# Kernel tuning notes

Measured on AMD Instinct MI355X. Metric: run time of the kernel, lower is better.

Reference implementation:

```python
import jax, jax.numpy as jnp
from jax import lax
import numpy as np

D = 8        # domain_num
L = 12       # label_num
C = 9        # attr_num
W = 128      # window_size
B = 4096
EPS = 1e-5


def setup_inputs() -> dict:
    key = jax.random.key(0)
    ks = jax.random.split(key, 12)
    s = 0.05
    return {
        "x": jax.random.normal(ks[0], (B, C, 1, W), dtype=jnp.float32),
        "weights": jax.random.uniform(ks[1], (B, D), dtype=jnp.float32),
        # per-domain stacked parameters (leading dim D)
        "gamma": jnp.ones((D, C), dtype=jnp.float32),
        "beta": jnp.zeros((D, C), dtype=jnp.float32),
        "w1": jax.random.normal(ks[2], (D, 32, C, 9), dtype=jnp.float32) * s,
        "b1": jax.random.normal(ks[3], (D, 32), dtype=jnp.float32) * s,
        "w2": jax.random.normal(ks[4], (D, 64, 32, 9), dtype=jnp.float32) * s,
        "b2": jax.random.normal(ks[5], (D, 64), dtype=jnp.float32) * s,
        "fcw": jax.random.normal(ks[6], (D, L, 64 * 26), dtype=jnp.float32) * s,
        "fcb": jax.random.normal(ks[7], (D, L), dtype=jnp.float32) * s,
    }


def _maxpool2(h):
    # MaxPool along width, kernel 2 stride 2 (height is 1 and already squeezed)
    b, c, w = h.shape
    return h.reshape(b, c, w // 2, 2).max(axis=-1)


def _branch(x3, gamma, beta, w1, b1, w2, b2, fcw, fcb):
    # x3: [B, C, W]. BatchNorm2d in training mode: batch stats over (N, H, W).
    mean = x3.mean(axis=(0, 2), keepdims=True)
    var = x3.var(axis=(0, 2), keepdims=True)
    xn = (x3 - mean) * lax.rsqrt(var + EPS) * gamma[None, :, None] + beta[None, :, None]
    dn = ('NCH', 'OIH', 'NCH')
    h = lax.conv_general_dilated(xn, w1, (1,), 'VALID', dimension_numbers=dn)
    h = _maxpool2(jax.nn.relu(h + b1[None, :, None]))          # [B,32,60]
    h = lax.conv_general_dilated(h, w2, (1,), 'VALID', dimension_numbers=dn)
    h = _maxpool2(jax.nn.relu(h + b2[None, :, None]))          # [B,64,26]
    flat = h.reshape(h.shape[0], 64 * 26)
    return jax.nn.relu(flat @ fcw.T + fcb)                      # [B,L]


def reference(x, weights, gamma, beta, w1, b1, w2, b2, fcw, fcb):
    x3 = x[:, :, 0, :]  # squeeze height=1 -> [B,C,W]
    per_domain = jax.vmap(_branch, in_axes=(None, 0, 0, 0, 0, 0, 0, 0, 0))(
        x3, gamma, beta, w1, b1, w2, b2, fcw, fcb)              # [D,B,L]
    # vectorized form of the nested python-loop weighted sum over domains
    return jnp.einsum('bd,dbl->bl', weights, per_domain)        # [B,L]
```

## Files before the change

kernel.cpp:

```cpp
#include <hip/hip_runtime.h>
#include <hip/hip_bf16.h>

#define D 8
#define L 12
#define C 9
#define W 128
#define B 4096
#define EPS 1e-5f

typedef __attribute__((ext_vector_type(8))) short v8s;
typedef __attribute__((ext_vector_type(4))) float v4f;

#define OFF_STATS 0
#define OFF_B1E   1152
#define OFF_W1T   1408
#define OFF_W2T   21888
#define OFF_FCWP  95616

#define REGION 2336

__device__ inline unsigned short f2bf(float f) {
    unsigned u = __builtin_bit_cast(unsigned, f);
    u += 0x7FFFu + ((u >> 16) & 1u);
    return (unsigned short)(u >> 16);
}
__device__ inline unsigned pk2(float a, float b) {
    float2 f2; f2.x = a; f2.y = b;
    __hip_bfloat162 h = __float22bfloat162_rn(f2);
    unsigned u; __builtin_memcpy(&u, &h, 4);
    return u;
}

__global__ void stats_repack_kernel(const float* __restrict__ x,
                                    const float* __restrict__ w2,
                                    const float* __restrict__ fcw,
                                    float* __restrict__ ws,
                                    float* __restrict__ out) {
    const int t = threadIdx.x;
    __shared__ float redS[8];
    if (blockIdx.x < 576) {
        const int c = blockIdx.x % 9;
        const int slice = blockIdx.x / 9;
        const int w4 = t & 31, br = t >> 5;
        const float4* x4 = (const float4*)x;
        float s = 0.f, s2 = 0.f;
        for (int b = slice * 8 + br; b < B; b += 64 * 8) {
            float4 v = x4[(size_t)b * 288 + c * 32 + w4];
            s  += v.x + v.y + v.z + v.w;
            s2 += v.x * v.x + v.y * v.y + v.z * v.z + v.w * v.w;
        }
        for (int off = 32; off >= 1; off >>= 1) {
            s  += __shfl_down(s, off);
            s2 += __shfl_down(s2, off);
        }
        if ((t & 63) == 0) { redS[(t >> 6) * 2] = s; redS[(t >> 6) * 2 + 1] = s2; }
        __syncthreads();
        if (t == 0) {
            ws[OFF_STATS + slice * 18 + c]     = redS[0] + redS[2] + redS[4] + redS[6];
            ws[OFF_STATS + slice * 18 + 9 + c] = redS[1] + redS[3] + redS[5] + redS[7];
        }
    } else if (blockIdx.x < 616) {
        const int i0 = blockIdx.x - 576;
        const int d = i0 / 5, part = i0 % 5;
        short* w2t  = (short*)(ws + OFF_W2T);
        short* fcwp = (short*)(ws + OFF_FCWP);
        if (part < 2) {
            for (int i = part * 256 + t; i < 64 * 9 * 32; i += 512) {
                int o = i / 288, r = i % 288, tap = r / 32, ic = r & 31;
                w2t[(size_t)d * 18432 + i] =
                    (short)f2bf(w2[(((size_t)(d * 64 + o)) * 32 + ic) * 9 + tap]);
            }
        } else {
            for (int i = (part - 2) * 256 + t; i < 12 * 1664; i += 768) {
                int l = i / 1664, k = i % 1664, p = k >> 6, o = k & 63;
                fcwp[((size_t)d * 12) * 1664 + i] =
                    (short)f2bf(fcw[((size_t)(d * 12 + l)) * 1664 + o * 26 + p]);
            }
        }
    } else {
        const int base = (blockIdx.x - 616) * 6144;
        float4 z; z.x = z.y = z.z = z.w = 0.f;
        float4* o4 = (float4*)(out + base);
        for (int i = t; i < 1536; i += 256) o4[i] = z;
    }
}

__global__ void fold1_kernel(const float* __restrict__ w1, const float* __restrict__ b1,
                             const float* __restrict__ gamma, const float* __restrict__ beta,
                             float* __restrict__ ws) {
    const int d = blockIdx.x, t = threadIdx.x;
    __shared__ float g[9], bt[9];
    if (t < 64) {
        for (int c = 0; c < 9; c++) {
            float s  = ws[OFF_STATS + t * 18 + c];
            float s2 = ws[OFF_STATS + t * 18 + 9 + c];
            for (int off = 32; off >= 1; off >>= 1) {
                s  += __shfl_down(s, off);
                s2 += __shfl_down(s2, off);
            }
            if (t == 0) {
                const float N = (float)B * (float)W;
                float m  = s / N;
                float vv = s2 / N - m * m;
                float inv = rsqrtf(vv + EPS);
                float gg = gamma[d * 9 + c] * inv;
                g[c] = gg; bt[c] = beta[d * 9 + c] - gg * m;
            }
        }
    }
    __syncthreads();
    const int o = t >> 3, sub = t & 7;
    short* w1t = (short*)(ws + OFF_W1T);
    short* dst = w1t + (size_t)d * 5120 + o * 160;
    const float* src = w1 + ((size_t)(d * 32 + o)) * 81;
    float bias_part = 0.f;
    for (int tap = sub; tap < 10; tap += 8) {
        for (int c = 0; c < 16; c++) {
            float v = 0.f;
            if (tap < 9 && c < 9) {
                float wv = src[c * 9 + tap];
                v = wv * g[c];
                bias_part += wv * bt[c];
            }
            dst[tap * 16 + c] = (short)f2bf(v);
        }
    }
    bias_part += __shfl_xor(bias_part, 1);
    bias_part += __shfl_xor(bias_part, 2);
    bias_part += __shfl_xor(bias_part, 4);
    if (sub == 0) ws[OFF_B1E + d * 32 + o] = b1[d * 32 + o] + bias_part;
}

__global__ __launch_bounds__(256, 4)
void branch_kernel(const float* __restrict__ x,
                   const float* __restrict__ b2g,
                   const float* __restrict__ fcb,
                   const float* __restrict__ wts,
                   const float* __restrict__ ws,
                   float* __restrict__ out) {
    const int t = threadIdx.x;
    const int lane = t & 63;
    const int wv = t >> 6;
    const int d = blockIdx.y;
    const int b0 = blockIdx.x * 4;
    const short* w1t  = (const short*)(ws + OFF_W1T) + (size_t)d * 5120;
    const short* w2t  = (const short*)(ws + OFF_W2T) + (size_t)d * 18432;
    const short* fcwp = (const short*)(ws + OFF_FCWP) + (size_t)d * 12 * 1664;
    const float* b1e  = ws + OFF_B1E + d * 32;

    __shared__ __align__(16) short lds[4 * REGION];
    short* myr = &lds[wv * REGION];

    const int n = lane & 15, quad = lane >> 4;

    {
        const float* xrow = x + (size_t)(b0 + wv) * 1152;
        #pragma unroll
        for (int rep = 0; rep < 2; rep++) {
            const int w = lane + rep * 64;
            float v[9];
            #pragma unroll
            for (int c = 0; c < 9; c++) v[c] = xrow[c * 128 + w];
            uint4 lo, hi;
            lo.x = pk2(v[0], v[1]); lo.y = pk2(v[2], v[3]);
            lo.z = pk2(v[4], v[5]); lo.w = pk2(v[6], v[7]);
            hi.x = (unsigned)(unsigned short)f2bf(v[8]); hi.y = 0; hi.z = 0; hi.w = 0;
            *(uint4*)&myr[(0 * 144 + w) * 8] = lo;
            *(uint4*)&myr[(1 * 144 + w) * 8] = hi;
        }
        if (lane < 16) {
            uint4 z; z.x = z.y = z.z = z.w = 0;
            *(uint4*)&myr[(0 * 144 + 128 + lane) * 8] = z;
            *(uint4*)&myr[(1 * 144 + 128 + lane) * 8] = z;
        }
    }

    {
        const int qh = quad >> 1, ql = quad & 1;
        const float bias0 = b1e[n], bias1 = b1e[16 + n];
        v4f acc[8][2];
        #pragma unroll
        for (int mt = 0; mt < 8; mt++)
            #pragma unroll
            for (int nt = 0; nt < 2; nt++) { v4f z = {0.f,0.f,0.f,0.f}; acc[mt][nt] = z; }
        #pragma unroll
        for (int s = 0; s < 5; s++) {
            v8s Bw0 = *(const v8s*)&w1t[n * 160 + (2 * s + qh) * 16 + ql * 8];
            v8s Bw1 = *(const v8s*)&w1t[(16 + n) * 160 + (2 * s + qh) * 16 + ql * 8];
            #pragma unroll
            for (int mt = 0; mt < 8; mt++) {
                const int row = mt * 16 + n + 2 * s + qh;
                v8s Af = *(const v8s*)&myr[(ql * 144 + row) * 8];
                acc[mt][0] = __builtin_amdgcn_mfma_f32_16x16x32_bf16(Af, Bw0, acc[mt][0], 0, 0, 0);
                acc[mt][1] = __builtin_amdgcn_mfma_f32_16x16x32_bf16(Af, Bw1, acc[mt][1], 0, 0, 0);
            }
        }
        unsigned held[16];
        #pragma unroll
        for (int mt = 0; mt < 8; mt++)
            #pragma unroll
            for (int nt = 0; nt < 2; nt++) {
                const float bb = nt ? bias1 : bias0;
                float h0  = fmaxf(fmaxf(acc[mt][nt][0], acc[mt][nt][1]) + bb, 0.f);
                float h1v = fmaxf(fmaxf(acc[mt][nt][2], acc[mt][nt][3]) + bb, 0.f);
                held[mt * 2 + nt] = pk2(h0, h1v);
            }
        #pragma unroll
        for (int mt = 0; mt < 8; mt++) {
            const int p = mt * 8 + quad * 2;
            #pragma unroll
            for (int nt = 0; nt < 2; nt++) {
                const unsigned pr = held[mt * 2 + nt];
                const int plane = nt * 2 + (n >> 3);
                const int col = n & 7;
                if (p < 60)     myr[(plane * 73 + p) * 8 + col]     = (short)(pr & 0xFFFFu);
                if (p + 1 < 60) myr[(plane * 73 + p + 1) * 8 + col] = (short)(pr >> 16);
            }
        }
    }

    {
        float biasv[4];
        #pragma unroll
        for (int nt = 0; nt < 4; nt++) biasv[nt] = b2g[d * 64 + nt * 16 + n];
        v4f acc[4][4];
        #pragma unroll
        for (int mt = 0; mt < 4; mt++)
            #pragma unroll
            for (int nt = 0; nt < 4; nt++) { v4f z = {0.f,0.f,0.f,0.f}; acc[mt][nt] = z; }
        for (int tap = 0; tap < 9; tap++) {
            v8s Bw[4];
            #pragma unroll
            for (int nt = 0; nt < 4; nt++)
                Bw[nt] = *(const v8s*)&w2t[(nt * 16 + n) * 288 + tap * 32 + quad * 8];
            #pragma unroll
            for (int mt = 0; mt < 4; mt++) {
                const int row = mt * 16 + n + tap;
                v8s Af = *(const v8s*)&myr[(quad * 73 + row) * 8];
                #pragma unroll
                for (int nt = 0; nt < 4; nt++)
                    acc[mt][nt] = __builtin_amdgcn_mfma_f32_16x16x32_bf16(Af, Bw[nt], acc[mt][nt], 0, 0, 0);
            }
        }
        unsigned held[16];
        #pragma unroll
        for (int mt = 0; mt < 4; mt++)
            #pragma unroll
            for (int nt = 0; nt < 4; nt++) {
                float h0  = fmaxf(fmaxf(acc[mt][nt][0], acc[mt][nt][1]) + biasv[nt], 0.f);
                float h1v = fmaxf(fmaxf(acc[mt][nt][2], acc[mt][nt][3]) + biasv[nt], 0.f);
                held[mt * 4 + nt] = pk2(h0, h1v);
            }
        #pragma unroll
        for (int mt = 0; mt < 4; mt++) {
            const int p = mt * 8 + quad * 2;
            #pragma unroll
            for (int nt = 0; nt < 4; nt++) {
                const unsigned pr = held[mt * 4 + nt];
                const int oc = nt * 16 + n;
                if (p < 26) {
                    const int gs = (oc >> 3) ^ (p & 7);
                    myr[p * 64 + gs * 8 + (oc & 7)] = (short)(pr & 0xFFFFu);
                }
                if (p + 1 < 26) {
                    const int gs = (oc >> 3) ^ ((p + 1) & 7);
                    myr[(p + 1) * 64 + gs * 8 + (oc & 7)] = (short)(pr >> 16);
                }
            }
        }
    }
    __syncthreads();

    {
        const int lrow = (n < 12) ? n : 0;
        v4f acc = {0.f, 0.f, 0.f, 0.f};
        for (int ks = wv; ks < 52; ks += 4) {
            const int p = ks >> 1;
            const int gs = ((ks & 1) * 4 + quad) ^ (p & 7);
            v8s A  = *(const v8s*)&fcwp[lrow * 1664 + ks * 32 + quad * 8];
            v8s Bf = *(const v8s*)&lds[(n & 3) * REGION + p * 64 + gs * 8];
            acc = __builtin_amdgcn_mfma_f32_16x16x32_bf16(A, Bf, acc, 0, 0, 0);
        }
        float* red = (float*)(myr + 1672);
        *(float4*)&red[lane * 4] = *(float4*)&acc;
    }
    __syncthreads();
    if (t < 64) {
        float sum[4] = {0.f, 0.f, 0.f, 0.f};
        #pragma unroll
        for (int w = 0; w < 4; w++) {
            const float* redw = (const float*)(&lds[w * REGION + 1672]);
            float4 v = *(const float4*)&redw[lane * 4];
            sum[0] += v.x; sum[1] += v.y; sum[2] += v.z; sum[3] += v.w;
        }
        if (n < 4) {
            const float wgt = wts[(size_t)(b0 + n) * 8 + d];
            #pragma unroll
            for (int r = 0; r < 4; r++) {
                const int l = quad * 4 + r;
                if (l < 12) {
                    float v = fmaxf(sum[r] + fcb[d * 12 + l], 0.f);
                    atomicAdd(&out[(size_t)(b0 + n) * 12 + l], wgt * v);
                }
            }
        }
    }
}

extern "C" void kernel_launch(void* const* d_in, const int* in_sizes, int n_in,
                              void* d_out, int out_size, void* d_ws, size_t ws_size,
                              hipStream_t stream) {
    const float* x       = (const float*)d_in[0];
    const float* weights = (const float*)d_in[1];
    const float* gamma   = (const float*)d_in[2];
    const float* beta    = (const float*)d_in[3];
    const float* w1      = (const float*)d_in[4];
    const float* b1      = (const float*)d_in[5];
    const float* w2      = (const float*)d_in[6];
    const float* b2      = (const float*)d_in[7];
    const float* fcw     = (const float*)d_in[8];
    const float* fcb     = (const float*)d_in[9];
    float* ws  = (float*)d_ws;
    float* out = (float*)d_out;

    stats_repack_kernel<<<dim3(624), 256, 0, stream>>>(x, w2, fcw, ws, out);
    fold1_kernel<<<dim3(D), 256, 0, stream>>>(w1, b1, gamma, beta, ws);
    branch_kernel<<<dim3(B / 4, D), 256, 0, stream>>>(x, b2, fcb, weights, ws, out);
}
```

Before: 234.6 us.

## Split each sample across two waves and halve samples per block

Each block now handles 2 samples instead of 4. Two waves share one sample and split the conv1 and conv2 M-tiles between them, with block barriers added between stages. Layer-1 output goes to a separate LDS offset so the two waves can share it. The grid doubles, per-wave accumulator register pressure roughly halves, and launch bounds rise to 5 blocks per CU to raise occupancy and latency hiding. In exchange there are extra __syncthreads and twice as many per-sample weight fragment loads.

```diff
diff --git a/kernel.cpp b/kernel.cpp
--- a/kernel.cpp
+++ b/kernel.cpp
@@ -17,7 +17,8 @@
 #define OFF_W2T   21888
 #define OFF_FCWP  95616
 
-#define REGION 2336
+#define REGION 4640
+#define H1OFF  2304
 
 __device__ inline unsigned short f2bf(float f) {
     unsigned u = __builtin_bit_cast(unsigned, f);
@@ -131,7 +132,7 @@
     if (sub == 0) ws[OFF_B1E + d * 32 + o] = b1[d * 32 + o] + bias_part;
 }
 
-__global__ __launch_bounds__(256, 4)
+__global__ __launch_bounds__(256, 5)
 void branch_kernel(const float* __restrict__ x,
                    const float* __restrict__ b2g,
                    const float* __restrict__ fcb,
@@ -141,46 +142,46 @@
     const int t = threadIdx.x;
     const int lane = t & 63;
     const int wv = t >> 6;
+    const int r  = wv >> 1;
+    const int h  = wv & 1;
     const int d = blockIdx.y;
-    const int b0 = blockIdx.x * 4;
+    const int b0 = blockIdx.x * 2;
     const short* w1t  = (const short*)(ws + OFF_W1T) + (size_t)d * 5120;
     const short* w2t  = (const short*)(ws + OFF_W2T) + (size_t)d * 18432;
     const short* fcwp = (const short*)(ws + OFF_FCWP) + (size_t)d * 12 * 1664;
     const float* b1e  = ws + OFF_B1E + d * 32;
 
-    __shared__ __align__(16) short lds[4 * REGION];
-    short* myr = &lds[wv * REGION];
+    __shared__ __align__(16) short lds[2 * REGION];
+    short* myrow = &lds[r * REGION];
 
     const int n = lane & 15, quad = lane >> 4;
 
     {
-        const float* xrow = x + (size_t)(b0 + wv) * 1152;
-        #pragma unroll
-        for (int rep = 0; rep < 2; rep++) {
-            const int w = lane + rep * 64;
-            float v[9];
-            #pragma unroll
-            for (int c = 0; c < 9; c++) v[c] = xrow[c * 128 + w];
-            uint4 lo, hi;
-            lo.x = pk2(v[0], v[1]); lo.y = pk2(v[2], v[3]);
-            lo.z = pk2(v[4], v[5]); lo.w = pk2(v[6], v[7]);
-            hi.x = (unsigned)(unsigned short)f2bf(v[8]); hi.y = 0; hi.z = 0; hi.w = 0;
-            *(uint4*)&myr[(0 * 144 + w) * 8] = lo;
-            *(uint4*)&myr[(1 * 144 + w) * 8] = hi;
-        }
-        if (lane < 16) {
+        const float* xrow = x + (size_t)(b0 + r) * 1152;
+        const int w = lane + h * 64;
+        float v[9];
+        #pragma unroll
+        for (int c = 0; c < 9; c++) v[c] = xrow[c * 128 + w];
+        uint4 lo, hi;
+        lo.x = pk2(v[0], v[1]); lo.y = pk2(v[2], v[3]);
+        lo.z = pk2(v[4], v[5]); lo.w = pk2(v[6], v[7]);
+        hi.x = (unsigned)(unsigned short)f2bf(v[8]); hi.y = 0; hi.z = 0; hi.w = 0;
+        *(uint4*)&myrow[(0 * 144 + w) * 8] = lo;
+        *(uint4*)&myrow[(1 * 144 + w) * 8] = hi;
+        if (h == 0 && lane < 16) {
             uint4 z; z.x = z.y = z.z = z.w = 0;
-            *(uint4*)&myr[(0 * 144 + 128 + lane) * 8] = z;
-            *(uint4*)&myr[(1 * 144 + 128 + lane) * 8] = z;
-        }
-    }
+            *(uint4*)&myrow[(0 * 144 + 128 + lane) * 8] = z;
+            *(uint4*)&myrow[(1 * 144 + 128 + lane) * 8] = z;
+        }
+    }
+    __syncthreads();
 
     {
         const int qh = quad >> 1, ql = quad & 1;
         const float bias0 = b1e[n], bias1 = b1e[16 + n];
-        v4f acc[8][2];
-        #pragma unroll
-        for (int mt = 0; mt < 8; mt++)
+        v4f acc[4][2];
+        #pragma unroll
+        for (int mt = 0; mt < 4; mt++)
             #pragma unroll
             for (int nt = 0; nt < 2; nt++) { v4f z = {0.f,0.f,0.f,0.f}; acc[mt][nt] = z; }
         #pragma unroll
@@ -188,16 +189,16 @@
             v8s Bw0 = *(const v8s*)&w1t[n * 160 + (2 * s + qh) * 16 + ql * 8];
             v8s Bw1 = *(const v8s*)&w1t[(16 + n) * 160 + (2 * s + qh) * 16 + ql * 8];
             #pragma unroll
-            for (int mt = 0; mt < 8; mt++) {
-                const int row = mt * 16 + n + 2 * s + qh;
-                v8s Af = *(const v8s*)&myr[(ql * 144 + row) * 8];
+            for (int mt = 0; mt < 4; mt++) {
+                const int row = (h * 4 + mt) * 16 + n + 2 * s + qh;
+                v8s Af = *(const v8s*)&myrow[(ql * 144 + row) * 8];
                 acc[mt][0] = __builtin_amdgcn_mfma_f32_16x16x32_bf16(Af, Bw0, acc[mt][0], 0, 0, 0);
                 acc[mt][1] = __builtin_amdgcn_mfma_f32_16x16x32_bf16(Af, Bw1, acc[mt][1], 0, 0, 0);
             }
         }
-        unsigned held[16];
-        #pragma unroll
-        for (int mt = 0; mt < 8; mt++)
+        unsigned held[8];
+        #pragma unroll
+        for (int mt = 0; mt < 4; mt++)
             #pragma unroll
             for (int nt = 0; nt < 2; nt++) {
                 const float bb = nt ? bias1 : bias0;
@@ -206,26 +207,27 @@
                 held[mt * 2 + nt] = pk2(h0, h1v);
             }
         #pragma unroll
-        for (int mt = 0; mt < 8; mt++) {
-            const int p = mt * 8 + quad * 2;
+        for (int mt = 0; mt < 4; mt++) {
+            const int p = (h * 4 + mt) * 8 + quad * 2;
             #pragma unroll
             for (int nt = 0; nt < 2; nt++) {
                 const unsigned pr = held[mt * 2 + nt];
                 const int plane = nt * 2 + (n >> 3);
                 const int col = n & 7;
-                if (p < 60)     myr[(plane * 73 + p) * 8 + col]     = (short)(pr & 0xFFFFu);
-                if (p + 1 < 60) myr[(plane * 73 + p + 1) * 8 + col] = (short)(pr >> 16);
-            }
-        }
-    }
+                if (p < 60)     myrow[H1OFF + (plane * 73 + p) * 8 + col]     = (short)(pr & 0xFFFFu);
+                if (p + 1 < 60) myrow[H1OFF + (plane * 73 + p + 1) * 8 + col] = (short)(pr >> 16);
+            }
+        }
+    }
+    __syncthreads();
 
     {
         float biasv[4];
         #pragma unroll
         for (int nt = 0; nt < 4; nt++) biasv[nt] = b2g[d * 64 + nt * 16 + n];
-        v4f acc[4][4];
-        #pragma unroll
-        for (int mt = 0; mt < 4; mt++)
+        v4f acc[2][4];
+        #pragma unroll
+        for (int mt = 0; mt < 2; mt++)
             #pragma unroll
             for (int nt = 0; nt < 4; nt++) { v4f z = {0.f,0.f,0.f,0.f}; acc[mt][nt] = z; }
         for (int tap = 0; tap < 9; tap++) {
@@ -234,17 +236,17 @@
             for (int nt = 0; nt < 4; nt++)
                 Bw[nt] = *(const v8s*)&w2t[(nt * 16 + n) * 288 + tap * 32 + quad * 8];
             #pragma unroll
-            for (int mt = 0; mt < 4; mt++) {
-                const int row = mt * 16 + n + tap;
-                v8s Af = *(const v8s*)&myr[(quad * 73 + row) * 8];
+            for (int mt = 0; mt < 2; mt++) {
+                const int row = (h * 2 + mt) * 16 + n + tap;
+                v8s Af = *(const v8s*)&myrow[H1OFF + (quad * 73 + row) * 8];
                 #pragma unroll
                 for (int nt = 0; nt < 4; nt++)
                     acc[mt][nt] = __builtin_amdgcn_mfma_f32_16x16x32_bf16(Af, Bw[nt], acc[mt][nt], 0, 0, 0);
             }
         }
-        unsigned held[16];
-        #pragma unroll
-        for (int mt = 0; mt < 4; mt++)
+        unsigned held[8];
+        #pragma unroll
+        for (int mt = 0; mt < 2; mt++)
             #pragma unroll
             for (int nt = 0; nt < 4; nt++) {
                 float h0  = fmaxf(fmaxf(acc[mt][nt][0], acc[mt][nt][1]) + biasv[nt], 0.f);
@@ -252,19 +254,19 @@
                 held[mt * 4 + nt] = pk2(h0, h1v);
             }
         #pragma unroll
-        for (int mt = 0; mt < 4; mt++) {
-            const int p = mt * 8 + quad * 2;
+        for (int mt = 0; mt < 2; mt++) {
+            const int p = (h * 2 + mt) * 8 + quad * 2;
             #pragma unroll
             for (int nt = 0; nt < 4; nt++) {
                 const unsigned pr = held[mt * 4 + nt];
                 const int oc = nt * 16 + n;
                 if (p < 26) {
                     const int gs = (oc >> 3) ^ (p & 7);
-                    myr[p * 64 + gs * 8 + (oc & 7)] = (short)(pr & 0xFFFFu);
+                    myrow[p * 64 + gs * 8 + (oc & 7)] = (short)(pr & 0xFFFFu);
                 }
                 if (p + 1 < 26) {
                     const int gs = (oc >> 3) ^ ((p + 1) & 7);
-                    myr[(p + 1) * 64 + gs * 8 + (oc & 7)] = (short)(pr >> 16);
+                    myrow[(p + 1) * 64 + gs * 8 + (oc & 7)] = (short)(pr >> 16);
                 }
             }
         }
@@ -278,28 +280,28 @@
             const int p = ks >> 1;
             const int gs = ((ks & 1) * 4 + quad) ^ (p & 7);
             v8s A  = *(const v8s*)&fcwp[lrow * 1664 + ks * 32 + quad * 8];
-            v8s Bf = *(const v8s*)&lds[(n & 3) * REGION + p * 64 + gs * 8];
+            v8s Bf = *(const v8s*)&lds[(n & 1) * REGION + p * 64 + gs * 8];
             acc = __builtin_amdgcn_mfma_f32_16x16x32_bf16(A, Bf, acc, 0, 0, 0);
         }
-        float* red = (float*)(myr + 1672);
-        *(float4*)&red[lane * 4] = *(float4*)&acc;
+        float* red = (float*)&lds[r * REGION + H1OFF];
+        *(float4*)&red[(h * 256) + lane * 4] = *(float4*)&acc;
     }
     __syncthreads();
     if (t < 64) {
         float sum[4] = {0.f, 0.f, 0.f, 0.f};
         #pragma unroll
         for (int w = 0; w < 4; w++) {
-            const float* redw = (const float*)(&lds[w * REGION + 1672]);
-            float4 v = *(const float4*)&redw[lane * 4];
+            const float* redw = (const float*)&lds[(w >> 1) * REGION + H1OFF];
+            float4 v = *(const float4*)&redw[((w & 1) * 256) + lane * 4];
             sum[0] += v.x; sum[1] += v.y; sum[2] += v.z; sum[3] += v.w;
         }
-        if (n < 4) {
+        if (n < 2) {
             const float wgt = wts[(size_t)(b0 + n) * 8 + d];
             #pragma unroll
-            for (int r = 0; r < 4; r++) {
-                const int l = quad * 4 + r;
+            for (int r4 = 0; r4 < 4; r4++) {
+                const int l = quad * 4 + r4;
                 if (l < 12) {
-                    float v = fmaxf(sum[r] + fcb[d * 12 + l], 0.f);
+                    float v = fmaxf(sum[r4] + fcb[d * 12 + l], 0.f);
                     atomicAdd(&out[(size_t)(b0 + n) * 12 + l], wgt * v);
                 }
             }
@@ -325,5 +327,5 @@
 
     stats_repack_kernel<<<dim3(624), 256, 0, stream>>>(x, w2, fcw, ws, out);
     fold1_kernel<<<dim3(D), 256, 0, stream>>>(w1, b1, gamma, beta, ws);
-    branch_kernel<<<dim3(B / 4, D), 256, 0, stream>>>(x, b2, fcb, weights, ws, out);
-}
+    branch_kernel<<<dim3(B / 2, D), 256, 0, stream>>>(x, b2, fcb, weights, ws, out);
+}
```

After: 344.8 us. 1.47x slower.
